# Kernel optimization log

Measured on AMD Instinct MI355X. Metric: run time of the kernel, lower is better.

Reference implementation:

```python
import jax, jax.numpy as jnp
import numpy as np

B, N_IN, N_OUT = 8192, 2048, 2048


def setup_inputs() -> dict:
    key = jax.random.key(0)
    kx, kw = jax.random.split(key)
    x = jax.random.normal(kx, (B, N_IN), dtype=jnp.float32)
    # torch: uniform_(-0.5, 0.5)
    weight = jax.random.uniform(kw, (N_IN, N_OUT), dtype=jnp.float32, minval=-0.5, maxval=0.5)
    return {"x": x, "weight": weight}


def reference(x, weight):
    # Binarize: W > 0 -> {0, 1}; then dense matmul (batch, n_in) @ (n_in, n_out)
    w_bin = (weight > 0).astype(x.dtype)
    return x @ w_bin
```

## Files before the change

kernel.cpp:

```cpp
#include <hip/hip_runtime.h>


#define MDIM 8192
#define NDIM 2048
#define KDIM 2048
#define NT   (KDIM / 128)
#define CH   (64 * KDIM)

typedef __attribute__((ext_vector_type(8))) short short8;
typedef __attribute__((ext_vector_type(4))) float float4v;
typedef __attribute__((ext_vector_type(4))) float f32x4;
typedef __attribute__((ext_vector_type(4))) int int4v;
typedef __attribute__((ext_vector_type(4))) unsigned short ushort4v;
typedef __attribute__((ext_vector_type(8))) unsigned short ushort8v;

__device__ __forceinline__ unsigned short f2bf(float f) {
    union { float f; unsigned u; } v; v.f = f;
    unsigned r = v.u + 0x7FFFu + ((v.u >> 16) & 1u);
    return (unsigned short)(r >> 16);
}

__device__ __forceinline__ void gload_lds16(void* l, const void* g) {
    __builtin_amdgcn_global_load_lds(
        (const __attribute__((address_space(1))) unsigned int*)g,
        (__attribute__((address_space(3))) unsigned int*)l,
        16, 0, 0);
}

#define FENCE asm volatile("" ::: "memory")
#define BAR do { FENCE; __builtin_amdgcn_s_barrier(); FENCE; } while (0)

__global__ __launch_bounds__(256) void prep(const float* __restrict__ X,
                                            const float* __restrict__ W,
                                            signed char* __restrict__ Xq,
                                            signed char* __restrict__ Wt,
                                            float* __restrict__ Sc) {
    __shared__ __align__(16) signed char T[64][80];
    __shared__ float wm[4];
    const int t = threadIdx.x;
    const int bid = blockIdx.x;

    if (bid < MDIM) {
        const int row = bid;
        const float* xr = X + (size_t)row * KDIM + t * 8;
        float4v a = *reinterpret_cast<const float4v*>(xr);
        float4v b = *reinterpret_cast<const float4v*>(xr + 4);
        float m = fabsf(a[0]);
        m = fmaxf(m, fabsf(a[1])); m = fmaxf(m, fabsf(a[2])); m = fmaxf(m, fabsf(a[3]));
        m = fmaxf(m, fabsf(b[0])); m = fmaxf(m, fabsf(b[1]));
        m = fmaxf(m, fabsf(b[2])); m = fmaxf(m, fabsf(b[3]));
#pragma unroll
        for (int off = 32; off; off >>= 1)
            m = fmaxf(m, __shfl_xor(m, off));
        if ((t & 63) == 0) wm[t >> 6] = m;
        __syncthreads();
        const float s = fmaxf(fmaxf(wm[0], wm[1]), fmaxf(wm[2], wm[3]));
        const float inv = (s > 0.f) ? 127.0f / s : 0.f;

        int q[8];
        q[0] = __float2int_rn(a[0] * inv); q[1] = __float2int_rn(a[1] * inv);
        q[2] = __float2int_rn(a[2] * inv); q[3] = __float2int_rn(a[3] * inv);
        q[4] = __float2int_rn(b[0] * inv); q[5] = __float2int_rn(b[1] * inv);
        q[6] = __float2int_rn(b[2] * inv); q[7] = __float2int_rn(b[3] * inv);
        unsigned lo = (q[0] & 255) | ((q[1] & 255) << 8) | ((q[2] & 255) << 16) | ((unsigned)(q[3] & 255) << 24);
        unsigned hi = (q[4] & 255) | ((q[5] & 255) << 8) | ((q[6] & 255) << 16) | ((unsigned)(q[7] & 255) << 24);
        unsigned* dst = (unsigned*)(Xq + (size_t)row * KDIM + t * 8);
        dst[0] = lo; dst[1] = hi;
        if (t == 0) Sc[row] = s * (1.0f / 127.0f);
    } else {
        const int wb = bid - MDIM;
        const int k0 = (wb >> 5) * 64;
        const int n0 = (wb & 31) * 64;
        const int kr = t >> 4;
        const int nc = (t & 15) * 4;
#pragma unroll
        for (int rr = 0; rr < 4; ++rr) {
            int k = k0 + rr * 16 + kr;
            float4v w4 = *reinterpret_cast<const float4v*>(W + (size_t)k * NDIM + n0 + nc);
#pragma unroll
            for (int c = 0; c < 4; ++c)
                T[nc + c][rr * 16 + kr] = (w4[c] > 0.0f) ? (signed char)1 : (signed char)0;
        }
        __syncthreads();
        const int row = t >> 2, ch = t & 3;
        int4v v = *reinterpret_cast<const int4v*>(&T[row][ch * 16]);
        *reinterpret_cast<int4v*>(Wt + (size_t)(n0 + row) * KDIM + k0 + ch * 16) = v;
    }
}

__global__ __launch_bounds__(512, 2) void gemm_i8(const signed char* __restrict__ A,
                                                  const signed char* __restrict__ Bt,
                                                  const float* __restrict__ Sc,
                                                  float* __restrict__ O) {
    extern __shared__ char lds[];
    const int tid  = threadIdx.x;
    const int lane = tid & 63;
    const int w    = tid >> 6;
    const int wr   = w >> 2;
    const int wc   = w & 3;

    int id  = blockIdx.x;
    int swz = (id & 7) * 32 + (id >> 3);
    const int bm = swz >> 3;
    const int bn = swz & 7;

    const int l3 = lane >> 3, l7 = lane & 7;
    const int srcOff = (w * 8 + l3) * KDIM + ((l7 ^ l3) << 4);
    const char* gA = (const char*)A + (size_t)(bm * 256) * KDIM + srcOff;
    const char* gB = (const char*)Bt + (size_t)(bn * 256) * KDIM + srcOff;

    const int fr = lane & 15, fg = lane >> 4;
    const int se0 = ((fg)     ^ (fr & 7)) << 4;
    const int se1 = ((4 + fg) ^ (fr & 7)) << 4;
    const int aRd = (wr * 128 + fr) * 128;
    const int bRd = 32768 + (wc * 64 + fr) * 128;

    int4v acc[8][4];
#pragma unroll
    for (int i = 0; i < 8; ++i)
#pragma unroll
        for (int j = 0; j < 4; ++j) {
            acc[i][j][0] = 0; acc[i][j][1] = 0; acc[i][j][2] = 0; acc[i][j][3] = 0;
        }

    gload_lds16(lds + 32768 + 0 * 8192 + w * 1024, gB + 0 * CH);
    gload_lds16(lds + 32768 + 1 * 8192 + w * 1024, gB + 1 * CH);
    gload_lds16(lds + 32768 + 2 * 8192 + w * 1024, gB + 2 * CH);
    gload_lds16(lds + 32768 + 3 * 8192 + w * 1024, gB + 3 * CH);
    gload_lds16(lds + 0 * 8192 + w * 1024, gA + 0 * CH);
    gload_lds16(lds + 1 * 8192 + w * 1024, gA + 1 * CH);
    gload_lds16(lds + 2 * 8192 + w * 1024, gA + 2 * CH);
    gload_lds16(lds + 3 * 8192 + w * 1024, gA + 3 * CH);

    for (int t = 0; t < NT; ++t) {
        const int cur = (t & 1) << 16;
        const int nxt = ((t + 1) & 1) << 16;
        const bool more = (t + 1 < NT);
        const char* gAs = gA + (size_t)(t + 1) * 128;
        const char* gBs = gB + (size_t)(t + 1) * 128;

        asm volatile("s_waitcnt vmcnt(0)" ::: "memory");
        BAR;

        if (more) {
            gload_lds16(lds + nxt + 32768 + 0 * 8192 + w * 1024, gBs + 0 * CH);
            gload_lds16(lds + nxt + 32768 + 1 * 8192 + w * 1024, gBs + 1 * CH);
            gload_lds16(lds + nxt + 32768 + 2 * 8192 + w * 1024, gBs + 2 * CH);
            gload_lds16(lds + nxt + 32768 + 3 * 8192 + w * 1024, gBs + 3 * CH);
            gload_lds16(lds + nxt + 0 * 8192 + w * 1024, gAs + 0 * CH);
            gload_lds16(lds + nxt + 1 * 8192 + w * 1024, gAs + 1 * CH);
            gload_lds16(lds + nxt + 2 * 8192 + w * 1024, gAs + 2 * CH);
            gload_lds16(lds + nxt + 3 * 8192 + w * 1024, gAs + 3 * CH);
        }

        int4v bfr[4][2], a01[2][2], a23[2][2], a45[2][2], a67[2][2];
#pragma unroll
        for (int n = 0; n < 4; ++n) {
            bfr[n][0] = *reinterpret_cast<const int4v*>(lds + cur + bRd + n * 2048 + se0);
            bfr[n][1] = *reinterpret_cast<const int4v*>(lds + cur + bRd + n * 2048 + se1);
        }
#pragma unroll
        for (int d = 0; d < 2; ++d) {
            a01[d][0] = *reinterpret_cast<const int4v*>(lds + cur + aRd + d * 2048 + se0);
            a01[d][1] = *reinterpret_cast<const int4v*>(lds + cur + aRd + d * 2048 + se1);
        }
#pragma unroll
        for (int d = 0; d < 2; ++d) {
            a23[d][0] = *reinterpret_cast<const int4v*>(lds + cur + aRd + (2 + d) * 2048 + se0);
            a23[d][1] = *reinterpret_cast<const int4v*>(lds + cur + aRd + (2 + d) * 2048 + se1);
        }
        __builtin_amdgcn_s_setprio(1);
#pragma unroll
        for (int d = 0; d < 2; ++d)
#pragma unroll
            for (int ni = 0; ni < 4; ++ni) {
                acc[d][ni] = __builtin_amdgcn_mfma_i32_16x16x64_i8(a01[d][0], bfr[ni][0], acc[d][ni], 0, 0, 0);
                acc[d][ni] = __builtin_amdgcn_mfma_i32_16x16x64_i8(a01[d][1], bfr[ni][1], acc[d][ni], 0, 0, 0);
            }
        __builtin_amdgcn_s_setprio(0);
#pragma unroll
        for (int d = 0; d < 2; ++d) {
            a45[d][0] = *reinterpret_cast<const int4v*>(lds + cur + aRd + (4 + d) * 2048 + se0);
            a45[d][1] = *reinterpret_cast<const int4v*>(lds + cur + aRd + (4 + d) * 2048 + se1);
        }
        __builtin_amdgcn_s_setprio(1);
#pragma unroll
        for (int d = 0; d < 2; ++d)
#pragma unroll
            for (int ni = 0; ni < 4; ++ni) {
                acc[2 + d][ni] = __builtin_amdgcn_mfma_i32_16x16x64_i8(a23[d][0], bfr[ni][0], acc[2 + d][ni], 0, 0, 0);
                acc[2 + d][ni] = __builtin_amdgcn_mfma_i32_16x16x64_i8(a23[d][1], bfr[ni][1], acc[2 + d][ni], 0, 0, 0);
            }
        __builtin_amdgcn_s_setprio(0);
#pragma unroll
        for (int d = 0; d < 2; ++d) {
            a67[d][0] = *reinterpret_cast<const int4v*>(lds + cur + aRd + (6 + d) * 2048 + se0);
            a67[d][1] = *reinterpret_cast<const int4v*>(lds + cur + aRd + (6 + d) * 2048 + se1);
        }
        __builtin_amdgcn_s_setprio(1);
#pragma unroll
        for (int d = 0; d < 2; ++d)
#pragma unroll
            for (int ni = 0; ni < 4; ++ni) {
                acc[4 + d][ni] = __builtin_amdgcn_mfma_i32_16x16x64_i8(a45[d][0], bfr[ni][0], acc[4 + d][ni], 0, 0, 0);
                acc[4 + d][ni] = __builtin_amdgcn_mfma_i32_16x16x64_i8(a45[d][1], bfr[ni][1], acc[4 + d][ni], 0, 0, 0);
            }
#pragma unroll
        for (int d = 0; d < 2; ++d)
#pragma unroll
            for (int ni = 0; ni < 4; ++ni) {
                acc[6 + d][ni] = __builtin_amdgcn_mfma_i32_16x16x64_i8(a67[d][0], bfr[ni][0], acc[6 + d][ni], 0, 0, 0);
                acc[6 + d][ni] = __builtin_amdgcn_mfma_i32_16x16x64_i8(a67[d][1], bfr[ni][1], acc[6 + d][ni], 0, 0, 0);
            }
        __builtin_amdgcn_s_setprio(0);
    }

    const int orow0 = bm * 256 + wr * 128 + fg * 4;
    const int ocol0 = bn * 256 + wc * 64 + fr;
#pragma unroll
    for (int mi = 0; mi < 8; ++mi)
#pragma unroll
        for (int r = 0; r < 4; ++r) {
            const int row = orow0 + mi * 16 + r;
            const float s = Sc[row];
            float* op = O + (size_t)row * NDIM + ocol0;
#pragma unroll
            for (int ni = 0; ni < 4; ++ni)
                op[ni * 16] = s * (float)acc[mi][ni][r];
        }
}

__global__ __launch_bounds__(256, 2) void binlin_fused(
        const float* __restrict__ X, const float* __restrict__ W,
        float* __restrict__ O) {
    const int tid = threadIdx.x;
    const int lane = tid & 63;
    const int wave = tid >> 6;
    const int wr = wave >> 1, wc = wave & 1;
    const int NWG = (MDIM / 128) * (NDIM / 128);
    int id = blockIdx.x;
    int swz = (id & 7) * (NWG >> 3) + (id >> 3);
    const int bm = swz >> 4, bn = swz & 15;

    __shared__ __align__(16) unsigned short As[128][40];
    __shared__ __align__(16) unsigned short Bs[128][40];

    const int rA = tid >> 3, kA = (tid & 7) * 4;
    const float* aPtr = X + (size_t)(bm * 128 + rA) * KDIM + kA;
    const int nB = (tid & 31) * 4, kB = (tid >> 5) * 4;
    const float* bPtr = W + (size_t)kB * NDIM + (size_t)bn * 128 + nB;

    float4v aReg[4], bReg[4];
#pragma unroll
    for (int p = 0; p < 4; ++p)
        aReg[p] = *reinterpret_cast<const float4v*>(aPtr + (size_t)(32 * p) * KDIM);
#pragma unroll
    for (int dk = 0; dk < 4; ++dk)
        bReg[dk] = *reinterpret_cast<const float4v*>(bPtr + (size_t)dk * NDIM);

    f32x4 acc[4][4];
#pragma unroll
    for (int i = 0; i < 4; ++i)
#pragma unroll
        for (int j = 0; j < 4; ++j) {
            acc[i][j][0] = 0.f; acc[i][j][1] = 0.f; acc[i][j][2] = 0.f; acc[i][j][3] = 0.f;
        }

    const int r16 = lane & 15, g8 = (lane >> 4) * 8;
    for (int kt = 0; kt < KDIM; kt += 32) {
#pragma unroll
        for (int p = 0; p < 4; ++p) {
            ushort4v v;
            v[0] = f2bf(aReg[p][0]); v[1] = f2bf(aReg[p][1]);
            v[2] = f2bf(aReg[p][2]); v[3] = f2bf(aReg[p][3]);
            *reinterpret_cast<ushort4v*>(&As[rA + 32 * p][kA]) = v;
        }
        unsigned short bb[4][4];
#pragma unroll
        for (int dk = 0; dk < 4; ++dk)
#pragma unroll
            for (int dn = 0; dn < 4; ++dn)
                bb[dn][dk] = (bReg[dk][dn] > 0.0f) ? (unsigned short)0x3F80u
                                                   : (unsigned short)0u;
#pragma unroll
        for (int dn = 0; dn < 4; ++dn) {
            ushort4v v;
            v[0] = bb[dn][0]; v[1] = bb[dn][1]; v[2] = bb[dn][2]; v[3] = bb[dn][3];
            *reinterpret_cast<ushort4v*>(&Bs[nB + dn][kB]) = v;
        }
        __syncthreads();
        if (kt + 32 < KDIM) {
#pragma unroll
            for (int p = 0; p < 4; ++p)
                aReg[p] = *reinterpret_cast<const float4v*>(
                    aPtr + (size_t)(32 * p) * KDIM + (kt + 32));
#pragma unroll
            for (int dk = 0; dk < 4; ++dk)
                bReg[dk] = *reinterpret_cast<const float4v*>(
                    bPtr + (size_t)(kt + 32 + dk) * NDIM);
        }
        short8 af[4], bf[4];
#pragma unroll
        for (int mi = 0; mi < 4; ++mi)
            af[mi] = *reinterpret_cast<const short8*>(&As[wr * 64 + mi * 16 + r16][g8]);
#pragma unroll
        for (int ni = 0; ni < 4; ++ni)
            bf[ni] = *reinterpret_cast<const short8*>(&Bs[wc * 64 + ni * 16 + r16][g8]);
#pragma unroll
        for (int mi = 0; mi < 4; ++mi)
#pragma unroll
            for (int ni = 0; ni < 4; ++ni)
                acc[mi][ni] = __builtin_amdgcn_mfma_f32_16x16x32_bf16(
                    af[mi], bf[ni], acc[mi][ni], 0, 0, 0);
        __syncthreads();
    }

    const int orow0 = bm * 128 + wr * 64 + (lane >> 4) * 4;
    const int ocol0 = bn * 128 + wc * 64 + r16;
#pragma unroll
    for (int mi = 0; mi < 4; ++mi)
#pragma unroll
        for (int ni = 0; ni < 4; ++ni)
#pragma unroll
            for (int r = 0; r < 4; ++r)
                O[(size_t)(orow0 + mi * 16 + r) * NDIM + ocol0 + ni * 16] =
                    acc[mi][ni][r];
}

extern "C" void kernel_launch(void* const* d_in, const int* in_sizes, int n_in,
                              void* d_out, int out_size, void* d_ws, size_t ws_size,
                              hipStream_t stream) {
    const float* X = (const float*)d_in[0];
    const float* W = (const float*)d_in[1];
    float* O = (float*)d_out;
    (void)in_sizes; (void)n_in; (void)out_size;

    const size_t xq_bytes = (size_t)MDIM * KDIM;
    const size_t wt_bytes = (size_t)NDIM * KDIM;
    const size_t sc_bytes = (size_t)MDIM * sizeof(float);
    const size_t need = xq_bytes + wt_bytes + sc_bytes;

    if (ws_size >= need) {
        signed char* Xq = (signed char*)d_ws;
        signed char* Wt = Xq + xq_bytes;
        float* Sc = (float*)(Wt + wt_bytes);
        hipFuncSetAttribute((const void*)gemm_i8,
                            hipFuncAttributeMaxDynamicSharedMemorySize, 131072);
        prep<<<dim3(MDIM + (KDIM / 64) * (NDIM / 64)), dim3(256), 0, stream>>>(X, W, Xq, Wt, Sc);
        gemm_i8<<<dim3((MDIM / 256) * (NDIM / 256)), dim3(512), 131072, stream>>>(Xq, Wt, Sc, O);
    } else {
        binlin_fused<<<dim3((MDIM / 128) * (NDIM / 128)), dim3(256), 0, stream>>>(X, W, O);
    }
}
```

Before: 56.10 us.

## Load binary weight fragments directly into registers, staging only activations in LDS

```diff
diff --git a/kernel.cpp b/kernel.cpp
--- a/kernel.cpp
+++ b/kernel.cpp
@@ -88,7 +88,7 @@
     }
 }
 
-__global__ __launch_bounds__(512, 2) void gemm_i8(const signed char* __restrict__ A,
+__global__ __launch_bounds__(512, 1) void gemm_bd(const signed char* __restrict__ A,
                                                   const signed char* __restrict__ Bt,
                                                   const float* __restrict__ Sc,
                                                   float* __restrict__ O) {
@@ -107,13 +107,13 @@
     const int l3 = lane >> 3, l7 = lane & 7;
     const int srcOff = (w * 8 + l3) * KDIM + ((l7 ^ l3) << 4);
     const char* gA = (const char*)A + (size_t)(bm * 256) * KDIM + srcOff;
-    const char* gB = (const char*)Bt + (size_t)(bn * 256) * KDIM + srcOff;
 
     const int fr = lane & 15, fg = lane >> 4;
     const int se0 = ((fg)     ^ (fr & 7)) << 4;
     const int se1 = ((4 + fg) ^ (fr & 7)) << 4;
     const int aRd = (wr * 128 + fr) * 128;
-    const int bRd = 32768 + (wc * 64 + fr) * 128;
+
+    const char* gBf = (const char*)Bt + (size_t)(bn * 256 + wc * 64 + fr) * KDIM + fg * 16;
 
     int4v acc[8][4];
 #pragma unroll
@@ -123,42 +123,33 @@
             acc[i][j][0] = 0; acc[i][j][1] = 0; acc[i][j][2] = 0; acc[i][j][3] = 0;
         }
 
-    gload_lds16(lds + 32768 + 0 * 8192 + w * 1024, gB + 0 * CH);
-    gload_lds16(lds + 32768 + 1 * 8192 + w * 1024, gB + 1 * CH);
-    gload_lds16(lds + 32768 + 2 * 8192 + w * 1024, gB + 2 * CH);
-    gload_lds16(lds + 32768 + 3 * 8192 + w * 1024, gB + 3 * CH);
-    gload_lds16(lds + 0 * 8192 + w * 1024, gA + 0 * CH);
-    gload_lds16(lds + 1 * 8192 + w * 1024, gA + 1 * CH);
-    gload_lds16(lds + 2 * 8192 + w * 1024, gA + 2 * CH);
-    gload_lds16(lds + 3 * 8192 + w * 1024, gA + 3 * CH);
+#pragma unroll
+    for (int c = 0; c < 4; ++c)
+        gload_lds16(lds + c * 8192 + w * 1024, gA + (size_t)c * CH);
+    int4v bf[4][2], bfn[4][2];
+#pragma unroll
+    for (int ni = 0; ni < 4; ++ni)
+#pragma unroll
+        for (int ks = 0; ks < 2; ++ks)
+            bf[ni][ks] = *reinterpret_cast<const int4v*>(
+                gBf + (size_t)ni * 16 * KDIM + ks * 64);
 
     for (int t = 0; t < NT; ++t) {
-        const int cur = (t & 1) << 16;
-        const int nxt = ((t + 1) & 1) << 16;
+        const int cur = (t & 1) << 15;
+        const int nxt = ((t + 1) & 1) << 15;
         const bool more = (t + 1 < NT);
-        const char* gAs = gA + (size_t)(t + 1) * 128;
-        const char* gBs = gB + (size_t)(t + 1) * 128;
+        const char* aN = gA + (size_t)(t + 1) * 128;
 
         asm volatile("s_waitcnt vmcnt(0)" ::: "memory");
         BAR;
 
         if (more) {
-            gload_lds16(lds + nxt + 32768 + 0 * 8192 + w * 1024, gBs + 0 * CH);
-            gload_lds16(lds + nxt + 32768 + 1 * 8192 + w * 1024, gBs + 1 * CH);
-            gload_lds16(lds + nxt + 32768 + 2 * 8192 + w * 1024, gBs + 2 * CH);
-            gload_lds16(lds + nxt + 32768 + 3 * 8192 + w * 1024, gBs + 3 * CH);
-            gload_lds16(lds + nxt + 0 * 8192 + w * 1024, gAs + 0 * CH);
-            gload_lds16(lds + nxt + 1 * 8192 + w * 1024, gAs + 1 * CH);
-            gload_lds16(lds + nxt + 2 * 8192 + w * 1024, gAs + 2 * CH);
-            gload_lds16(lds + nxt + 3 * 8192 + w * 1024, gAs + 3 * CH);
-        }
-
-        int4v bfr[4][2], a01[2][2], a23[2][2], a45[2][2], a67[2][2];
-#pragma unroll
-        for (int n = 0; n < 4; ++n) {
-            bfr[n][0] = *reinterpret_cast<const int4v*>(lds + cur + bRd + n * 2048 + se0);
-            bfr[n][1] = *reinterpret_cast<const int4v*>(lds + cur + bRd + n * 2048 + se1);
-        }
+#pragma unroll
+            for (int c = 0; c < 4; ++c)
+                gload_lds16(lds + nxt + c * 8192 + w * 1024, aN + (size_t)c * CH);
+        }
+
+        int4v a01[2][2], a23[2][2], a45[2][2], a67[2][2];
 #pragma unroll
         for (int d = 0; d < 2; ++d) {
             a01[d][0] = *reinterpret_cast<const int4v*>(lds + cur + aRd + d * 2048 + se0);
@@ -169,13 +160,22 @@
             a23[d][0] = *reinterpret_cast<const int4v*>(lds + cur + aRd + (2 + d) * 2048 + se0);
             a23[d][1] = *reinterpret_cast<const int4v*>(lds + cur + aRd + (2 + d) * 2048 + se1);
         }
+        if (more) {
+            const char* bN = gBf + (size_t)(t + 1) * 128;
+#pragma unroll
+            for (int ni = 0; ni < 4; ++ni)
+#pragma unroll
+                for (int ks = 0; ks < 2; ++ks)
+                    bfn[ni][ks] = *reinterpret_cast<const int4v*>(
+                        bN + (size_t)ni * 16 * KDIM + ks * 64);
+        }
         __builtin_amdgcn_s_setprio(1);
 #pragma unroll
         for (int d = 0; d < 2; ++d)
 #pragma unroll
             for (int ni = 0; ni < 4; ++ni) {
-                acc[d][ni] = __builtin_amdgcn_mfma_i32_16x16x64_i8(a01[d][0], bfr[ni][0], acc[d][ni], 0, 0, 0);
-                acc[d][ni] = __builtin_amdgcn_mfma_i32_16x16x64_i8(a01[d][1], bfr[ni][1], acc[d][ni], 0, 0, 0);
+                acc[d][ni] = __builtin_amdgcn_mfma_i32_16x16x64_i8(a01[d][0], bf[ni][0], acc[d][ni], 0, 0, 0);
+                acc[d][ni] = __builtin_amdgcn_mfma_i32_16x16x64_i8(a01[d][1], bf[ni][1], acc[d][ni], 0, 0, 0);
             }
         __builtin_amdgcn_s_setprio(0);
 #pragma unroll
@@ -188,8 +188,8 @@
         for (int d = 0; d < 2; ++d)
 #pragma unroll
             for (int ni = 0; ni < 4; ++ni) {
-                acc[2 + d][ni] = __builtin_amdgcn_mfma_i32_16x16x64_i8(a23[d][0], bfr[ni][0], acc[2 + d][ni], 0, 0, 0);
-                acc[2 + d][ni] = __builtin_amdgcn_mfma_i32_16x16x64_i8(a23[d][1], bfr[ni][1], acc[2 + d][ni], 0, 0, 0);
+                acc[2 + d][ni] = __builtin_amdgcn_mfma_i32_16x16x64_i8(a23[d][0], bf[ni][0], acc[2 + d][ni], 0, 0, 0);
+                acc[2 + d][ni] = __builtin_amdgcn_mfma_i32_16x16x64_i8(a23[d][1], bf[ni][1], acc[2 + d][ni], 0, 0, 0);
             }
         __builtin_amdgcn_s_setprio(0);
 #pragma unroll
@@ -202,17 +202,26 @@
         for (int d = 0; d < 2; ++d)
 #pragma unroll
             for (int ni = 0; ni < 4; ++ni) {
-                acc[4 + d][ni] = __builtin_amdgcn_mfma_i32_16x16x64_i8(a45[d][0], bfr[ni][0], acc[4 + d][ni], 0, 0, 0);
-                acc[4 + d][ni] = __builtin_amdgcn_mfma_i32_16x16x64_i8(a45[d][1], bfr[ni][1], acc[4 + d][ni], 0, 0, 0);
+                acc[4 + d][ni] = __builtin_amdgcn_mfma_i32_16x16x64_i8(a45[d][0], bf[ni][0], acc[4 + d][ni], 0, 0, 0);
+                acc[4 + d][ni] = __builtin_amdgcn_mfma_i32_16x16x64_i8(a45[d][1], bf[ni][1], acc[4 + d][ni], 0, 0, 0);
             }
 #pragma unroll
         for (int d = 0; d < 2; ++d)
 #pragma unroll
             for (int ni = 0; ni < 4; ++ni) {
-                acc[6 + d][ni] = __builtin_amdgcn_mfma_i32_16x16x64_i8(a67[d][0], bfr[ni][0], acc[6 + d][ni], 0, 0, 0);
-                acc[6 + d][ni] = __builtin_amdgcn_mfma_i32_16x16x64_i8(a67[d][1], bfr[ni][1], acc[6 + d][ni], 0, 0, 0);
+                acc[6 + d][ni] = __builtin_amdgcn_mfma_i32_16x16x64_i8(a67[d][0], bf[ni][0], acc[6 + d][ni], 0, 0, 0);
+                acc[6 + d][ni] = __builtin_amdgcn_mfma_i32_16x16x64_i8(a67[d][1], bf[ni][1], acc[6 + d][ni], 0, 0, 0);
             }
         __builtin_amdgcn_s_setprio(0);
+        FENCE;
+
+        if (more) {
+#pragma unroll
+            for (int ni = 0; ni < 4; ++ni)
+#pragma unroll
+                for (int ks = 0; ks < 2; ++ks)
+                    bf[ni][ks] = bfn[ni][ks];
+        }
     }
 
     const int orow0 = bm * 256 + wr * 128 + fg * 4;
@@ -299,19 +308,19 @@
                 bReg[dk] = *reinterpret_cast<const float4v*>(
                     bPtr + (size_t)(kt + 32 + dk) * NDIM);
         }
-        short8 af[4], bf[4];
+        short8 af[4], bfv[4];
 #pragma unroll
         for (int mi = 0; mi < 4; ++mi)
             af[mi] = *reinterpret_cast<const short8*>(&As[wr * 64 + mi * 16 + r16][g8]);
 #pragma unroll
         for (int ni = 0; ni < 4; ++ni)
-            bf[ni] = *reinterpret_cast<const short8*>(&Bs[wc * 64 + ni * 16 + r16][g8]);
+            bfv[ni] = *reinterpret_cast<const short8*>(&Bs[wc * 64 + ni * 16 + r16][g8]);
 #pragma unroll
         for (int mi = 0; mi < 4; ++mi)
 #pragma unroll
             for (int ni = 0; ni < 4; ++ni)
                 acc[mi][ni] = __builtin_amdgcn_mfma_f32_16x16x32_bf16(
-                    af[mi], bf[ni], acc[mi][ni], 0, 0, 0);
+                    af[mi], bfv[ni], acc[mi][ni], 0, 0, 0);
         __syncthreads();
     }
 
@@ -344,10 +353,10 @@
         signed char* Xq = (signed char*)d_ws;
         signed char* Wt = Xq + xq_bytes;
         float* Sc = (float*)(Wt + wt_bytes);
-        hipFuncSetAttribute((const void*)gemm_i8,
-                            hipFuncAttributeMaxDynamicSharedMemorySize, 131072);
+        hipFuncSetAttribute((const void*)gemm_bd,
+                            hipFuncAttributeMaxDynamicSharedMemorySize, 65536);
         prep<<<dim3(MDIM + (KDIM / 64) * (NDIM / 64)), dim3(256), 0, stream>>>(X, W, Xq, Wt, Sc);
-        gemm_i8<<<dim3((MDIM / 256) * (NDIM / 256)), dim3(512), 131072, stream>>>(Xq, Wt, Sc, O);
+        gemm_bd<<<dim3((MDIM / 256) * (NDIM / 256)), dim3(512), 65536, stream>>>(Xq, Wt, Sc, O);
     } else {
         binlin_fused<<<dim3((MDIM / 128) * (NDIM / 128)), dim3(256), 0, stream>>>(X, W, O);
     }
```

Result: slower. 71.58 us (+27.6%).
